# Performance work log

Hardware: AMD Instinct MI355X
Metric: run time of the kernel (lower is better)

## Reference

```python
import jax, jax.numpy as jnp
import numpy as np


def setup_inputs() -> dict:
    key = jax.random.key(0)
    ks = jax.random.split(key, 8)
    B, T, U = 4, 256, 64
    A, D, H, V = 512, 640, 640, 1024
    inp = {
        "encoder_output": jax.random.normal(ks[0], (B, T, A), dtype=jnp.float32),
        "decoder_output": jax.random.normal(ks[1], (B, U, D), dtype=jnp.float32),
        "W_enc": jax.random.normal(ks[2], (A, H), dtype=jnp.float32) / np.sqrt(A),
        "b_enc": jnp.zeros((H,), dtype=jnp.float32),
        "W_dec": jax.random.normal(ks[3], (D, H), dtype=jnp.float32) / np.sqrt(D),
        "b_dec": jnp.zeros((H,), dtype=jnp.float32),
        "W_out": jax.random.normal(ks[4], (H, V), dtype=jnp.float32) / np.sqrt(H),
        "b_out": jnp.zeros((V,), dtype=jnp.float32),
    }
    return inp


def reference(encoder_output, decoder_output, W_enc, b_enc, W_dec, b_dec, W_out, b_out):
    # project encoder (B,T,A)->(B,T,H) and decoder (B,U,D)->(B,U,H)
    enc = encoder_output @ W_enc + b_enc
    dec = decoder_output @ W_dec + b_dec
    # broadcast-add to (B,T,U,H), tanh, project to vocab, log-softmax
    z = jnp.tanh(enc[:, :, None, :] + dec[:, None, :, :])
    logits = z @ W_out + b_out  # (B,T,U,V)
    return jax.nn.log_softmax(logits, axis=-1)
```

## Files before the change

kernel.cpp:

```cpp
#include <hip/hip_runtime.h>
#include <hip/hip_bf16.h>
#include <cstdint>

#define BB 4
#define TT 256
#define UB 64
#define AA 512
#define DD 640
#define HH 640
#define VV 1024

typedef __attribute__((ext_vector_type(8))) short short8;
typedef __attribute__((ext_vector_type(4))) float f32x4;

__device__ __forceinline__ unsigned short f2bf(float f) {
    unsigned u = __builtin_bit_cast(unsigned, f);
    u += 0x7fffu + ((u >> 16) & 1u);
    return (unsigned short)(u >> 16);
}

__device__ __forceinline__ float fast_tanh(float x) {
    return 1.0f - 2.0f / (1.0f + __expf(2.0f * x));
}

__global__ __launch_bounds__(256) void kpack(const float* __restrict__ W,
                                             unsigned short* __restrict__ wp) {
    __shared__ float tile[32][64];
    const int kb  = blockIdx.x >> 4;
    const int nbg = blockIdx.x & 15;
    const int tid = threadIdx.x;
#pragma unroll
    for (int i = 0; i < 8; ++i) {
        int idx = tid + (i << 8);
        int r = idx >> 6, c = idx & 63;
        tile[r][c] = W[(size_t)(kb * 32 + r) * VV + nbg * 64 + c];
    }
    __syncthreads();
    const int hi  = tid & 3;
    const int np  = (tid >> 2) & 15;
    const int nbl = tid >> 6;
    __align__(16) unsigned short v[8];
#pragma unroll
    for (int j = 0; j < 8; ++j)
        v[j] = f2bf(tile[hi * 8 + j][nbl * 16 + np]);
    size_t off = (size_t)((kb * 64 + nbg * 4 + nbl) * 512 + np * 32 + hi * 8);
    *reinterpret_cast<uint4*>(wp + off) = *reinterpret_cast<const uint4*>(v);
}

__global__ __launch_bounds__(256) void kproj(
    const float* __restrict__ enc_in, const float* __restrict__ dec_in,
    const float* __restrict__ We, const float* __restrict__ be,
    const float* __restrict__ Wd, const float* __restrict__ bd,
    float* __restrict__ enc_out, float* __restrict__ dec_out) {
    __shared__ float As[16][68];
    __shared__ float Bs[16][68];
    const int bi = blockIdx.x;
    const float *A, *W, *bias;
    float* C;
    int K, bm, bn;
    if (bi < 160) { A = enc_in; W = We; bias = be; C = enc_out; K = AA; bm = bi / 10; bn = bi - bm * 10; }
    else { int bj = bi - 160; A = dec_in; W = Wd; bias = bd; C = dec_out; K = DD; bm = bj / 10; bn = bj - bm * 10; }
    const int tid  = threadIdx.x;
    const int row0 = bm * 64, n0 = bn * 64;
    const int tm = tid & 15, tn = tid >> 4;
    const int am = tid & 63, akq = tid >> 6;
    const int bk = tid >> 4, bn4 = (tid & 15) * 4;

    float acc[4][4] = {};
    float4 a4 = *reinterpret_cast<const float4*>(A + (size_t)(row0 + am) * K + akq * 4);
    float4 b4 = *reinterpret_cast<const float4*>(W + (size_t)bk * HH + n0 + bn4);

    for (int k0 = 0; k0 < K; k0 += 16) {
        As[akq * 4 + 0][am] = a4.x;
        As[akq * 4 + 1][am] = a4.y;
        As[akq * 4 + 2][am] = a4.z;
        As[akq * 4 + 3][am] = a4.w;
        *reinterpret_cast<float4*>(&Bs[bk][bn4]) = b4;
        __syncthreads();
        if (k0 + 16 < K) {
            a4 = *reinterpret_cast<const float4*>(A + (size_t)(row0 + am) * K + k0 + 16 + akq * 4);
            b4 = *reinterpret_cast<const float4*>(W + (size_t)(k0 + 16 + bk) * HH + n0 + bn4);
        }
#pragma unroll
        for (int kk = 0; kk < 16; ++kk) {
            float4 av = *reinterpret_cast<const float4*>(&As[kk][tm * 4]);
            float4 bv = *reinterpret_cast<const float4*>(&Bs[kk][tn * 4]);
            float a_[4] = {av.x, av.y, av.z, av.w};
            float b_[4] = {bv.x, bv.y, bv.z, bv.w};
#pragma unroll
            for (int i = 0; i < 4; ++i)
#pragma unroll
                for (int j = 0; j < 4; ++j)
                    acc[i][j] = fmaf(a_[i], b_[j], acc[i][j]);
        }
        __syncthreads();
    }
    float bv0 = bias[n0 + tn * 4 + 0], bv1 = bias[n0 + tn * 4 + 1];
    float bv2 = bias[n0 + tn * 4 + 2], bv3 = bias[n0 + tn * 4 + 3];
#pragma unroll
    for (int i = 0; i < 4; ++i) {
        float4 o = {acc[i][0] + bv0, acc[i][1] + bv1, acc[i][2] + bv2, acc[i][3] + bv3};
        *reinterpret_cast<float4*>(C + (size_t)(row0 + tm * 4 + i) * HH + n0 + tn * 4) = o;
    }
}

__global__ __launch_bounds__(512, 2) void kmain(
    const float* __restrict__ encp, const float* __restrict__ decp,
    const unsigned short* __restrict__ wp, const float* __restrict__ bo,
    float* __restrict__ out) {
    __shared__ __align__(16) unsigned char zb[UB * 640];
    __shared__ __align__(16) float red1[UB][8];
    __shared__ __align__(16) float red2[UB][8];
    const int bt   = blockIdx.x;
    const int b    = bt >> 8;
    const int tid  = threadIdx.x;
    const int lane = tid & 63;
    const int wv   = tid >> 6;
    const int lo   = lane & 15;
    const int hi   = lane >> 4;
    const float* encr = encp + (size_t)bt * HH;
    const float* decr = decp + (size_t)b * UB * HH;
    const int nb0 = wv * 8;

    f32x4 acc[4][8];
#pragma unroll
    for (int mf = 0; mf < 4; ++mf)
#pragma unroll
        for (int nf = 0; nf < 8; ++nf)
            acc[mf][nf] = (f32x4){0.f, 0.f, 0.f, 0.f};

#pragma unroll
    for (int half = 0; half < 2; ++half) {
#pragma unroll
        for (int i = 0; i < 5; ++i) {
            int c  = tid + i * 512;
            int u  = c / 40;
            int h0 = (c - u * 40) * 8;
            const float4* dp = reinterpret_cast<const float4*>(decr + (size_t)u * HH + half * 320 + h0);
            const float4* ep = reinterpret_cast<const float4*>(encr + half * 320 + h0);
            float4 d0 = dp[0], d1 = dp[1];
            float4 e0 = ep[0], e1 = ep[1];
            __align__(16) unsigned short zs[8];
            zs[0] = f2bf(fast_tanh(e0.x + d0.x));
            zs[1] = f2bf(fast_tanh(e0.y + d0.y));
            zs[2] = f2bf(fast_tanh(e0.z + d0.z));
            zs[3] = f2bf(fast_tanh(e0.w + d0.w));
            zs[4] = f2bf(fast_tanh(e1.x + d1.x));
            zs[5] = f2bf(fast_tanh(e1.y + d1.y));
            zs[6] = f2bf(fast_tanh(e1.z + d1.z));
            zs[7] = f2bf(fast_tanh(e1.w + d1.w));
            unsigned addr = (unsigned)(u * 640 + h0 * 2) ^ ((unsigned)(u & 7) << 4);
            *reinterpret_cast<uint4*>(zb + addr) = *reinterpret_cast<const uint4*>(zs);
        }
        __syncthreads();

#pragma unroll
        for (int kb = 0; kb < 10; ++kb) {
            const int kbg = half * 10 + kb;
            short8 af[4];
#pragma unroll
            for (int mf = 0; mf < 4; ++mf) {
                int row = mf * 16 + lo;
                unsigned addr = (unsigned)(row * 640 + kb * 64 + hi * 16) ^
                                ((unsigned)(row & 7) << 4);
                af[mf] = *reinterpret_cast<const short8*>(zb + addr);
            }
#pragma unroll
            for (int nf = 0; nf < 8; ++nf) {
                const unsigned short* p =
                    wp + (size_t)((kbg * 64 + nb0 + nf) * 512 + lo * 32 + hi * 8);
                short8 bf = *reinterpret_cast<const short8*>(p);
#pragma unroll
                for (int mf = 0; mf < 4; ++mf)
                    acc[mf][nf] = __builtin_amdgcn_mfma_f32_16x16x32_bf16(
                        af[mf], bf, acc[mf][nf], 0, 0, 0);
            }
        }
        __syncthreads();
    }

    const int n0 = wv * 128;
    float bbv[8];
#pragma unroll
    for (int nf = 0; nf < 8; ++nf) bbv[nf] = bo[n0 + nf * 16 + lo];
#pragma unroll
    for (int mf = 0; mf < 4; ++mf)
#pragma unroll
        for (int nf = 0; nf < 8; ++nf) {
            acc[mf][nf][0] += bbv[nf];
            acc[mf][nf][1] += bbv[nf];
            acc[mf][nf][2] += bbv[nf];
            acc[mf][nf][3] += bbv[nf];
        }

#pragma unroll
    for (int mf = 0; mf < 4; ++mf)
#pragma unroll
        for (int rg = 0; rg < 4; ++rg) {
            float v = acc[mf][0][rg];
#pragma unroll
            for (int nf = 1; nf < 8; ++nf) v = fmaxf(v, acc[mf][nf][rg]);
            v = fmaxf(v, __shfl_xor(v, 1));
            v = fmaxf(v, __shfl_xor(v, 2));
            v = fmaxf(v, __shfl_xor(v, 4));
            v = fmaxf(v, __shfl_xor(v, 8));
            if (lo == 0) red1[mf * 16 + hi * 4 + rg][wv] = v;
        }
    __syncthreads();
    float rmax[4][4];
#pragma unroll
    for (int mf = 0; mf < 4; ++mf)
#pragma unroll
        for (int rg = 0; rg < 4; ++rg) {
            int row = mf * 16 + hi * 4 + rg;
            const float4* r4 = reinterpret_cast<const float4*>(&red1[row][0]);
            float4 x = r4[0], y = r4[1];
            rmax[mf][rg] = fmaxf(fmaxf(fmaxf(x.x, x.y), fmaxf(x.z, x.w)),
                                 fmaxf(fmaxf(y.x, y.y), fmaxf(y.z, y.w)));
        }
#pragma unroll
    for (int mf = 0; mf < 4; ++mf)
#pragma unroll
        for (int rg = 0; rg < 4; ++rg) {
            float s = 0.f;
#pragma unroll
            for (int nf = 0; nf < 8; ++nf)
                s += __expf(acc[mf][nf][rg] - rmax[mf][rg]);
            s += __shfl_xor(s, 1);
            s += __shfl_xor(s, 2);
            s += __shfl_xor(s, 4);
            s += __shfl_xor(s, 8);
            if (lo == 0) red2[mf * 16 + hi * 4 + rg][wv] = s;
        }
    __syncthreads();
    float lz[4][4];
#pragma unroll
    for (int mf = 0; mf < 4; ++mf)
#pragma unroll
        for (int rg = 0; rg < 4; ++rg) {
            int row = mf * 16 + hi * 4 + rg;
            const float4* r4 = reinterpret_cast<const float4*>(&red2[row][0]);
            float4 x = r4[0], y = r4[1];
            float s = (x.x + x.y) + (x.z + x.w) + (y.x + y.y) + (y.z + y.w);
            lz[mf][rg] = rmax[mf][rg] + __logf(s);
        }
    float* outbase = out + (size_t)bt * UB * VV;
#pragma unroll
    for (int mf = 0; mf < 4; ++mf)
#pragma unroll
        for (int rg = 0; rg < 4; ++rg) {
            int row = mf * 16 + hi * 4 + rg;
            float* orow = outbase + (size_t)row * VV + n0 + lo;
#pragma unroll
            for (int nf = 0; nf < 8; ++nf)
                orow[nf * 16] = acc[mf][nf][rg] - lz[mf][rg];
        }
}

extern "C" void kernel_launch(void* const* d_in, const int* in_sizes, int n_in,
                              void* d_out, int out_size, void* d_ws, size_t ws_size,
                              hipStream_t stream) {
    const float* enc_in = (const float*)d_in[0];
    const float* dec_in = (const float*)d_in[1];
    const float* We     = (const float*)d_in[2];
    const float* be     = (const float*)d_in[3];
    const float* Wd     = (const float*)d_in[4];
    const float* bd     = (const float*)d_in[5];
    const float* Wo     = (const float*)d_in[6];
    const float* bo     = (const float*)d_in[7];
    float* out = (float*)d_out;

    float* ws   = (float*)d_ws;
    float* encp = ws;
    float* decp = ws + 1024 * 640;
    unsigned short* wp = (unsigned short*)(ws + 1024 * 640 + 256 * 640);

    kpack<<<320, 256, 0, stream>>>(Wo, wp);
    kproj<<<200, 256, 0, stream>>>(enc_in, dec_in, We, be, Wd, bd, encp, decp);
    kmain<<<1024, 512, 0, stream>>>(encp, decp, wp, bo, out);
}
```

Baseline: 475.7 us.

## Merge prep kernels, widen main kernel to 1024 threads, nontemporal output stores

```diff
diff --git a/kernel.cpp b/kernel.cpp
--- a/kernel.cpp
+++ b/kernel.cpp
@@ -23,47 +23,50 @@
     return 1.0f - 2.0f / (1.0f + __expf(2.0f * x));
 }
 
-__global__ __launch_bounds__(256) void kpack(const float* __restrict__ W,
-                                             unsigned short* __restrict__ wp) {
-    __shared__ float tile[32][64];
-    const int kb  = blockIdx.x >> 4;
-    const int nbg = blockIdx.x & 15;
-    const int tid = threadIdx.x;
-#pragma unroll
-    for (int i = 0; i < 8; ++i) {
-        int idx = tid + (i << 8);
-        int r = idx >> 6, c = idx & 63;
-        tile[r][c] = W[(size_t)(kb * 32 + r) * VV + nbg * 64 + c];
-    }
-    __syncthreads();
-    const int hi  = tid & 3;
-    const int np  = (tid >> 2) & 15;
-    const int nbl = tid >> 6;
-    __align__(16) unsigned short v[8];
-#pragma unroll
-    for (int j = 0; j < 8; ++j)
-        v[j] = f2bf(tile[hi * 8 + j][nbl * 16 + np]);
-    size_t off = (size_t)((kb * 64 + nbg * 4 + nbl) * 512 + np * 32 + hi * 8);
-    *reinterpret_cast<uint4*>(wp + off) = *reinterpret_cast<const uint4*>(v);
-}
-
-__global__ __launch_bounds__(256) void kproj(
+__global__ __launch_bounds__(256) void kprep(
+    const float* __restrict__ W_out, unsigned short* __restrict__ wp,
     const float* __restrict__ enc_in, const float* __restrict__ dec_in,
     const float* __restrict__ We, const float* __restrict__ be,
     const float* __restrict__ Wd, const float* __restrict__ bd,
     float* __restrict__ enc_out, float* __restrict__ dec_out) {
-    __shared__ float As[16][68];
+    __shared__ float smem[16][137];
+    const int bi  = blockIdx.x;
+    const int tid = threadIdx.x;
+
+    if (bi < 320) {
+        float (*tile)[64] = reinterpret_cast<float (*)[64]>(&smem[0][0]);
+        const int kb  = bi >> 4;
+        const int nbg = bi & 15;
+#pragma unroll
+        for (int i = 0; i < 8; ++i) {
+            int idx = tid + (i << 8);
+            int r = idx >> 6, c = idx & 63;
+            tile[r][c] = W_out[(size_t)(kb * 32 + r) * VV + nbg * 64 + c];
+        }
+        __syncthreads();
+        const int hi  = tid & 3;
+        const int np  = (tid >> 2) & 15;
+        const int nbl = tid >> 6;
+        __align__(16) unsigned short v[8];
+#pragma unroll
+        for (int j = 0; j < 8; ++j)
+            v[j] = f2bf(tile[hi * 8 + j][nbl * 16 + np]);
+        size_t off = (size_t)((kb * 64 + nbg * 4 + nbl) * 512 + np * 32 + hi * 8);
+        *reinterpret_cast<uint4*>(wp + off) = *reinterpret_cast<const uint4*>(v);
+        return;
+    }
+
+    float (*As)[68] = reinterpret_cast<float (*)[68]>(&smem[0][0]);
     __shared__ float Bs[16][68];
-    const int bi = blockIdx.x;
+    const int bj = bi - 320;
     const float *A, *W, *bias;
     float* C;
     int K, bm, bn;
-    if (bi < 160) { A = enc_in; W = We; bias = be; C = enc_out; K = AA; bm = bi / 10; bn = bi - bm * 10; }
-    else { int bj = bi - 160; A = dec_in; W = Wd; bias = bd; C = dec_out; K = DD; bm = bj / 10; bn = bj - bm * 10; }
-    const int tid  = threadIdx.x;
+    if (bj < 160) { A = enc_in; W = We; bias = be; C = enc_out; K = AA; bm = bj / 10; bn = bj - bm * 10; }
+    else { int bq = bj - 160; A = dec_in; W = Wd; bias = bd; C = dec_out; K = DD; bm = bq / 10; bn = bq - bm * 10; }
     const int row0 = bm * 64, n0 = bn * 64;
     const int tm = tid & 15, tn = tid >> 4;
-    const int am = tid & 63, akq = tid >> 6;
+    const int am = tid >> 2, akq = tid & 3;
     const int bk = tid >> 4, bn4 = (tid & 15) * 4;
 
     float acc[4][4] = {};
@@ -104,11 +107,11 @@
     }
 }
 
-__global__ __launch_bounds__(512, 2) void kmain(
+__global__ __launch_bounds__(1024) void kmain(
     const float* __restrict__ encp, const float* __restrict__ decp,
     const unsigned short* __restrict__ wp, const float* __restrict__ bo,
     float* __restrict__ out) {
-    __shared__ __align__(16) unsigned char zb[UB * 640];
+    __shared__ __align__(16) unsigned char zb[UB * 1280];
     __shared__ __align__(16) float red1[UB][8];
     __shared__ __align__(16) float red2[UB][8];
     const int bt   = blockIdx.x;
@@ -116,85 +119,81 @@
     const int tid  = threadIdx.x;
     const int lane = tid & 63;
     const int wv   = tid >> 6;
+    const int cg   = wv & 7;
+    const int rg_g = wv >> 3;
     const int lo   = lane & 15;
     const int hi   = lane >> 4;
     const float* encr = encp + (size_t)bt * HH;
     const float* decr = decp + (size_t)b * UB * HH;
-    const int nb0 = wv * 8;
-
-    f32x4 acc[4][8];
-#pragma unroll
-    for (int mf = 0; mf < 4; ++mf)
+
+#pragma unroll
+    for (int i = 0; i < 5; ++i) {
+        int c  = tid + (i << 10);
+        int u  = c / 80;
+        int h0 = (c - u * 80) * 8;
+        const float4* dp = reinterpret_cast<const float4*>(decr + (size_t)u * HH + h0);
+        const float4* ep = reinterpret_cast<const float4*>(encr + h0);
+        float4 d0 = dp[0], d1 = dp[1];
+        float4 e0 = ep[0], e1 = ep[1];
+        __align__(16) unsigned short zs[8];
+        zs[0] = f2bf(fast_tanh(e0.x + d0.x));
+        zs[1] = f2bf(fast_tanh(e0.y + d0.y));
+        zs[2] = f2bf(fast_tanh(e0.z + d0.z));
+        zs[3] = f2bf(fast_tanh(e0.w + d0.w));
+        zs[4] = f2bf(fast_tanh(e1.x + d1.x));
+        zs[5] = f2bf(fast_tanh(e1.y + d1.y));
+        zs[6] = f2bf(fast_tanh(e1.z + d1.z));
+        zs[7] = f2bf(fast_tanh(e1.w + d1.w));
+        unsigned addr = (unsigned)(u * 1280 + h0 * 2) ^ ((unsigned)(u & 7) << 4);
+        *reinterpret_cast<uint4*>(zb + addr) = *reinterpret_cast<const uint4*>(zs);
+    }
+    __syncthreads();
+
+    f32x4 acc[2][8];
+#pragma unroll
+    for (int mf = 0; mf < 2; ++mf)
 #pragma unroll
         for (int nf = 0; nf < 8; ++nf)
             acc[mf][nf] = (f32x4){0.f, 0.f, 0.f, 0.f};
-
-#pragma unroll
-    for (int half = 0; half < 2; ++half) {
-#pragma unroll
-        for (int i = 0; i < 5; ++i) {
-            int c  = tid + i * 512;
-            int u  = c / 40;
-            int h0 = (c - u * 40) * 8;
-            const float4* dp = reinterpret_cast<const float4*>(decr + (size_t)u * HH + half * 320 + h0);
-            const float4* ep = reinterpret_cast<const float4*>(encr + half * 320 + h0);
-            float4 d0 = dp[0], d1 = dp[1];
-            float4 e0 = ep[0], e1 = ep[1];
-            __align__(16) unsigned short zs[8];
-            zs[0] = f2bf(fast_tanh(e0.x + d0.x));
-            zs[1] = f2bf(fast_tanh(e0.y + d0.y));
-            zs[2] = f2bf(fast_tanh(e0.z + d0.z));
-            zs[3] = f2bf(fast_tanh(e0.w + d0.w));
-            zs[4] = f2bf(fast_tanh(e1.x + d1.x));
-            zs[5] = f2bf(fast_tanh(e1.y + d1.y));
-            zs[6] = f2bf(fast_tanh(e1.z + d1.z));
-            zs[7] = f2bf(fast_tanh(e1.w + d1.w));
-            unsigned addr = (unsigned)(u * 640 + h0 * 2) ^ ((unsigned)(u & 7) << 4);
-            *reinterpret_cast<uint4*>(zb + addr) = *reinterpret_cast<const uint4*>(zs);
-        }
-        __syncthreads();
-
-#pragma unroll
-        for (int kb = 0; kb < 10; ++kb) {
-            const int kbg = half * 10 + kb;
-            short8 af[4];
-#pragma unroll
-            for (int mf = 0; mf < 4; ++mf) {
-                int row = mf * 16 + lo;
-                unsigned addr = (unsigned)(row * 640 + kb * 64 + hi * 16) ^
-                                ((unsigned)(row & 7) << 4);
-                af[mf] = *reinterpret_cast<const short8*>(zb + addr);
-            }
-#pragma unroll
-            for (int nf = 0; nf < 8; ++nf) {
-                const unsigned short* p =
-                    wp + (size_t)((kbg * 64 + nb0 + nf) * 512 + lo * 32 + hi * 8);
-                short8 bf = *reinterpret_cast<const short8*>(p);
-#pragma unroll
-                for (int mf = 0; mf < 4; ++mf)
-                    acc[mf][nf] = __builtin_amdgcn_mfma_f32_16x16x32_bf16(
-                        af[mf], bf, acc[mf][nf], 0, 0, 0);
-            }
-        }
-        __syncthreads();
-    }
-
-    const int n0 = wv * 128;
-    float bbv[8];
-#pragma unroll
-    for (int nf = 0; nf < 8; ++nf) bbv[nf] = bo[n0 + nf * 16 + lo];
-#pragma unroll
-    for (int mf = 0; mf < 4; ++mf)
+    const int nb0 = cg * 8;
+    const int r0  = rg_g * 32;
+#pragma unroll 4
+    for (int kb = 0; kb < 20; ++kb) {
+        short8 af[2];
+#pragma unroll
+        for (int mf = 0; mf < 2; ++mf) {
+            int row = r0 + mf * 16 + lo;
+            unsigned addr = (unsigned)(row * 1280 + kb * 64 + hi * 16) ^
+                            ((unsigned)(row & 7) << 4);
+            af[mf] = *reinterpret_cast<const short8*>(zb + addr);
+        }
 #pragma unroll
         for (int nf = 0; nf < 8; ++nf) {
-            acc[mf][nf][0] += bbv[nf];
-            acc[mf][nf][1] += bbv[nf];
-            acc[mf][nf][2] += bbv[nf];
-            acc[mf][nf][3] += bbv[nf];
-        }
-
-#pragma unroll
-    for (int mf = 0; mf < 4; ++mf)
+            const unsigned short* p =
+                wp + (size_t)((kb * 64 + nb0 + nf) * 512 + lo * 32 + hi * 8);
+            short8 bf = *reinterpret_cast<const short8*>(p);
+#pragma unroll
+            for (int mf = 0; mf < 2; ++mf)
+                acc[mf][nf] = __builtin_amdgcn_mfma_f32_16x16x32_bf16(
+                    af[mf], bf, acc[mf][nf], 0, 0, 0);
+        }
+    }
+
+    const int n0 = cg * 128;
+#pragma unroll
+    for (int nf = 0; nf < 8; ++nf) {
+        float bbv = bo[n0 + nf * 16 + lo];
+#pragma unroll
+        for (int mf = 0; mf < 2; ++mf) {
+            acc[mf][nf][0] += bbv;
+            acc[mf][nf][1] += bbv;
+            acc[mf][nf][2] += bbv;
+            acc[mf][nf][3] += bbv;
+        }
+    }
+
+#pragma unroll
+    for (int mf = 0; mf < 2; ++mf)
 #pragma unroll
         for (int rg = 0; rg < 4; ++rg) {
             float v = acc[mf][0][rg];
@@ -204,22 +203,22 @@
             v = fmaxf(v, __shfl_xor(v, 2));
             v = fmaxf(v, __shfl_xor(v, 4));
             v = fmaxf(v, __shfl_xor(v, 8));
-            if (lo == 0) red1[mf * 16 + hi * 4 + rg][wv] = v;
+            if (lo == 0) red1[r0 + mf * 16 + hi * 4 + rg][cg] = v;
         }
     __syncthreads();
-    float rmax[4][4];
-#pragma unroll
-    for (int mf = 0; mf < 4; ++mf)
-#pragma unroll
-        for (int rg = 0; rg < 4; ++rg) {
-            int row = mf * 16 + hi * 4 + rg;
+    float rmax[2][4];
+#pragma unroll
+    for (int mf = 0; mf < 2; ++mf)
+#pragma unroll
+        for (int rg = 0; rg < 4; ++rg) {
+            int row = r0 + mf * 16 + hi * 4 + rg;
             const float4* r4 = reinterpret_cast<const float4*>(&red1[row][0]);
             float4 x = r4[0], y = r4[1];
             rmax[mf][rg] = fmaxf(fmaxf(fmaxf(x.x, x.y), fmaxf(x.z, x.w)),
                                  fmaxf(fmaxf(y.x, y.y), fmaxf(y.z, y.w)));
         }
 #pragma unroll
-    for (int mf = 0; mf < 4; ++mf)
+    for (int mf = 0; mf < 2; ++mf)
 #pragma unroll
         for (int rg = 0; rg < 4; ++rg) {
             float s = 0.f;
@@ -230,15 +229,15 @@
             s += __shfl_xor(s, 2);
             s += __shfl_xor(s, 4);
             s += __shfl_xor(s, 8);
-            if (lo == 0) red2[mf * 16 + hi * 4 + rg][wv] = s;
+            if (lo == 0) red2[r0 + mf * 16 + hi * 4 + rg][cg] = s;
         }
     __syncthreads();
-    float lz[4][4];
-#pragma unroll
-    for (int mf = 0; mf < 4; ++mf)
-#pragma unroll
-        for (int rg = 0; rg < 4; ++rg) {
-            int row = mf * 16 + hi * 4 + rg;
+    float lz[2][4];
+#pragma unroll
+    for (int mf = 0; mf < 2; ++mf)
+#pragma unroll
+        for (int rg = 0; rg < 4; ++rg) {
+            int row = r0 + mf * 16 + hi * 4 + rg;
             const float4* r4 = reinterpret_cast<const float4*>(&red2[row][0]);
             float4 x = r4[0], y = r4[1];
             float s = (x.x + x.y) + (x.z + x.w) + (y.x + y.y) + (y.z + y.w);
@@ -246,14 +245,15 @@
         }
     float* outbase = out + (size_t)bt * UB * VV;
 #pragma unroll
-    for (int mf = 0; mf < 4; ++mf)
-#pragma unroll
-        for (int rg = 0; rg < 4; ++rg) {
-            int row = mf * 16 + hi * 4 + rg;
+    for (int mf = 0; mf < 2; ++mf)
+#pragma unroll
+        for (int rg = 0; rg < 4; ++rg) {
+            int row = r0 + mf * 16 + hi * 4 + rg;
             float* orow = outbase + (size_t)row * VV + n0 + lo;
 #pragma unroll
             for (int nf = 0; nf < 8; ++nf)
-                orow[nf * 16] = acc[mf][nf][rg] - lz[mf][rg];
+                __builtin_nontemporal_store(acc[mf][nf][rg] - lz[mf][rg],
+                                            orow + nf * 16);
         }
 }
 
@@ -275,7 +275,6 @@
     float* decp = ws + 1024 * 640;
     unsigned short* wp = (unsigned short*)(ws + 1024 * 640 + 256 * 640);
 
-    kpack<<<320, 256, 0, stream>>>(Wo, wp);
-    kproj<<<200, 256, 0, stream>>>(enc_in, dec_in, We, be, Wd, bd, encp, decp);
-    kmain<<<1024, 512, 0, stream>>>(encp, decp, wp, bo, out);
-}
+    kprep<<<520, 256, 0, stream>>>(Wo, wp, enc_in, dec_in, We, be, Wd, bd, encp, decp);
+    kmain<<<1024, 1024, 0, stream>>>(encp, decp, wp, bo, out);
+}
```

Result: slower. 511.6 us (+7.6%).
